# Performance work log

Measured on AMD Instinct MI355X. Metric: run time of the kernel, lower is better.

The kernel has to match this reference:

```python
import jax, jax.numpy as jnp
import numpy as np

E = 8            # num_experts
K = 2            # top-k
CF = 1.25        # capacity_factor
NOISE_STD = 1.0 / E   # noise_mult / num_experts


def setup_inputs() -> dict:
    key = jax.random.key(0)
    ks = jax.random.split(key, 4)
    B, S, D, H = 8, 1024, 768, 3072
    x = jax.random.normal(ks[0], (B, S, D), jnp.float32)
    router_w = jax.random.normal(ks[1], (D, E), jnp.float32) * 0.02
    fc1_w = jax.random.normal(ks[2], (E, D, H), jnp.float32) * 0.02
    fc1_b = jnp.zeros((E, H), jnp.float32)
    fc2_w = jax.random.normal(ks[3], (E, H, D), jnp.float32) * 0.02
    fc2_b = jnp.zeros((E, D), jnp.float32)
    return dict(x=x, router_w=router_w, fc1_w=fc1_w, fc1_b=fc1_b, fc2_w=fc2_w, fc2_b=fc2_b)


def reference(x, router_w, fc1_w, fc1_b, fc2_w, fc2_b):
    B, S, D = x.shape
    N = B * S
    A = N * K                                   # total (token, slot) assignments
    capacity = int(round(K * N * CF / E))
    x_flat = x.reshape(N, D)

    # ---- router (eval mode: no noise, no dropout) ----
    logits = (x_flat @ router_w).astype(jnp.float32)          # [N,E]
    clean_probs = jax.nn.softmax(logits, axis=-1)
    noisy_logits = logits
    noisy_probs = jax.nn.softmax(noisy_logits, axis=-1)
    topk_probs, topk_idx = jax.lax.top_k(noisy_probs, K)      # [N,K]
    topk_probs = topk_probs.astype(x.dtype)

    flat_e = topk_idx.reshape(-1)                             # [A]
    expert_counts = jax.ops.segment_sum(jnp.ones((A,), jnp.float32), flat_e, num_segments=E)

    # ---- aux losses ----
    importance = clean_probs.sum(0)
    mi = importance.mean()
    loss_importance = jnp.var(importance) / (mi * mi + 1e-6)
    # kthvalue(noisy_logits, E-K+1) == (E-K+1)-th smallest == sorted[:, E-K]
    threshold = jnp.sort(noisy_logits, axis=-1)[:, E - K][:, None]
    prob_selected = 1.0 - jax.scipy.stats.norm.cdf(threshold - logits, loc=0.0, scale=NOISE_STD)
    load = prob_selected.sum(0)
    ml = load.mean()
    loss_load = jnp.var(load) / (ml * ml + 1e-6)
    aux_loss = 0.5 * (loss_importance + loss_load)

    # ---- priority-based capacity dropping (vectorized over all assignments) ----
    priority = clean_probs.max(-1)                            # [N]
    tok = jnp.repeat(jnp.arange(N, dtype=jnp.int32), K)       # [A] token of each assignment
    kslot = jnp.tile(jnp.arange(K, dtype=jnp.int32), N)       # [A] which top-k slot
    score = priority[tok] - kslot.astype(jnp.float32)         # combined_scores = -k_idx + priority
    # group by expert (ascending), within expert sort by score descending
    sort_key = flat_e.astype(jnp.float32) * (K + 2) - score
    order = jnp.argsort(sort_key)
    e_sorted = flat_e[order]
    counts = jax.ops.segment_sum(jnp.ones((A,), jnp.int32), flat_e, num_segments=E)
    starts = jnp.cumsum(counts) - counts
    rank_sorted = jnp.arange(A, dtype=jnp.int32) - starts[e_sorted]   # position within expert group
    rank = jnp.zeros((A,), jnp.int32).at[order].set(rank_sorted)
    keep = rank < capacity
    dropped = jnp.sum(~keep).astype(jnp.int32)

    # ---- dispatch into fixed [E, capacity] buffer (overflow slot sliced off) ----
    pos = jnp.where(keep, flat_e * capacity + rank, E * capacity)
    dispatch_tok = jnp.zeros((E * capacity + 1,), jnp.int32).at[pos].set(tok)[:-1]
    w_flat = topk_probs.reshape(-1)
    weight_buf = jnp.zeros((E * capacity + 1,), x.dtype).at[pos].set(jnp.where(keep, w_flat, 0.0))[:-1]

    xe = x_flat[dispatch_tok].reshape(E, capacity, D)         # gather
    h = jax.nn.gelu(jnp.einsum('ecd,edh->ech', xe, fc1_w) + fc1_b[:, None, :], approximate=False)
    ye = jnp.einsum('ech,ehd->ecd', h, fc2_w) + fc2_b[:, None, :]
    weighted = ye * weight_buf.reshape(E, capacity, 1)
    # padded slots have weight 0 and token 0 -> contribute nothing
    out_flat = jnp.zeros((N, D), x.dtype).at[dispatch_tok].add(weighted.reshape(E * capacity, D))

    return out_flat.reshape(B, S, D), aux_loss, dropped, expert_counts
```

## Files before the change

### kernel.cpp

```cpp
#include <hip/hip_runtime.h>
#include <hip/hip_bf16.h>
#include <math.h>

#define NTOK 8192
#define DIM  768
#define HDIM 3072
#define NE   8
#define CAP  2560
#define AMAX 16384

typedef __bf16 bf16x8  __attribute__((ext_vector_type(8)));
typedef __bf16 bf16x2  __attribute__((ext_vector_type(2)));
typedef float  floatx4 __attribute__((ext_vector_type(4)));

typedef unsigned int u32_g __attribute__((address_space(1)));
typedef unsigned int u32_l __attribute__((address_space(3)));

__device__ __forceinline__ void gl_lds16(const void* g, void* l) {
  __builtin_amdgcn_global_load_lds((const u32_g*)g, (u32_l*)l, 16, 0, 0);
}

__device__ __forceinline__ float gelu_exact(float v) {
  float z = fabsf(v) * 0.7071067811865475f;
  float t = __builtin_amdgcn_rcpf(1.0f + 0.3275911f * z);
  float p = ((((1.061405429f * t - 1.453152027f) * t + 1.421413741f) * t
              - 0.284496736f) * t + 0.254829592f) * t;
  float e = 1.0f - p * __expf(-z * z);
  e = copysignf(e, v);
  return 0.5f * v * (1.0f + e);
}

__global__ __launch_bounds__(256) void transpose_conv2(
    const float* __restrict__ w1, const float* __restrict__ w2,
    __bf16* __restrict__ o1, __bf16* __restrict__ o2)
{
  const int which = blockIdx.z;
  const float* src = which ? w2 : w1;
  __bf16* dst = which ? o2 : o1;
  const int Kd = which ? HDIM : DIM;
  const int Nd = which ? DIM : HDIM;
  const int e = blockIdx.y;
  const int tilesK = Kd >> 6;
  const int bk = blockIdx.x % tilesK, bn = blockIdx.x / tilesK;
  __shared__ float T[64][65];
  const float* se = src + (size_t)e * Kd * Nd;
  const int k0 = bk * 64, n0 = bn * 64;
  const int tid = threadIdx.x;
#pragma unroll
  for (int it = 0; it < 16; ++it) {
    int flat = tid + it * 256;
    int kk = flat >> 6, nn = flat & 63;
    T[kk][nn] = se[(size_t)(k0 + kk) * Nd + n0 + nn];
  }
  __syncthreads();
  const int n = tid >> 2, kg = tid & 3;
  bf16x8 v0, v1;
#pragma unroll
  for (int q = 0; q < 8; ++q) v0[q] = (__bf16)T[kg * 16 + q][n];
#pragma unroll
  for (int q = 0; q < 8; ++q) v1[q] = (__bf16)T[kg * 16 + 8 + q][n];
  __bf16* de = dst + (size_t)e * Nd * Kd + (size_t)(n0 + n) * Kd + k0 + kg * 16;
  *(bf16x8*)(de) = v0;
  *(bf16x8*)(de + 8) = v1;
}

__global__ __launch_bounds__(256) void router_kernel(
    const float* __restrict__ x, const float* __restrict__ rw,
    int* __restrict__ list_len, double* __restrict__ imp, double* __restrict__ loadacc,
    int* __restrict__ aidx, float* __restrict__ keyarr, float* __restrict__ warr)
{
  __shared__ float Wl[NE * DIM];
  __shared__ int   lcount[NE], lbase[NE];
  __shared__ int   s_e[32][2], s_pos[32][2];
  __shared__ float s_key[32][2], s_w[32][2];
  const int tid = threadIdx.x;
  for (int i = tid; i < NE * DIM; i += 256) {
    int e = i / DIM, d = i - e * DIM;
    Wl[i] = rw[d * NE + e];
  }
  if (tid < NE) lcount[tid] = 0;
  __syncthreads();
  const int wave = tid >> 6, lane = tid & 63;
  double my_imp = 0.0, my_load = 0.0;

  for (int it = 0; it < 8; ++it) {
    const int t = wave * 8 + it;
    const int n = blockIdx.x * 32 + t;
    const float* xr = x + (size_t)n * DIM;
    float part[NE];
#pragma unroll
    for (int e = 0; e < NE; ++e) part[e] = 0.f;
#pragma unroll
    for (int c = 0; c < DIM / 64; ++c) {
      float xv = xr[c * 64 + lane];
#pragma unroll
      for (int e = 0; e < NE; ++e) part[e] += xv * Wl[e * DIM + c * 64 + lane];
    }
#pragma unroll
    for (int off = 32; off > 0; off >>= 1) {
#pragma unroll
      for (int e = 0; e < NE; ++e) part[e] += __shfl_xor(part[e], off);
    }
    int e0 = 0; float v0 = part[0];
#pragma unroll
    for (int e = 1; e < NE; ++e) if (part[e] > v0) { v0 = part[e]; e0 = e; }
    int e1 = -1; float v1 = -3.4e38f;
#pragma unroll
    for (int e = 0; e < NE; ++e) if (e != e0 && part[e] > v1) { v1 = part[e]; e1 = e; }

    float pexp[NE]; float s = 0.f;
#pragma unroll
    for (int e = 0; e < NE; ++e) { pexp[e] = expf(part[e] - v0); s += pexp[e]; }
    const float inv = 1.0f / s;
    const float pr = inv;
    float w1v = 0.f;
#pragma unroll
    for (int e = 0; e < NE; ++e) if (e == e1) w1v = pexp[e] * inv;

    float myl = 0.f, mypexp = 0.f;
#pragma unroll
    for (int e = 0; e < NE; ++e) if (lane == e) { myl = part[e]; mypexp = pexp[e]; }
    if (lane < NE) {
      my_imp  += (double)(mypexp * inv);
      my_load += (double)(0.5f * erfcf((v1 - myl) * 5.656854249492380f));
    }
    if (lane == 0) {
      int p0 = atomicAdd(&lcount[e0], 1);
      int p1 = atomicAdd(&lcount[e1], 1);
      s_e[t][0] = e0; s_pos[t][0] = p0;
      s_key[t][0] = (float)(e0 * 4) - pr;
      s_w[t][0] = pr;
      s_e[t][1] = e1; s_pos[t][1] = p1;
      s_key[t][1] = (float)(e1 * 4) - (pr - 1.0f);
      s_w[t][1] = w1v;
    }
  }
  __syncthreads();
  if (tid < NE) lbase[tid] = atomicAdd(&list_len[tid], lcount[tid]);
  __syncthreads();
  if (tid < 64) {
    const int t = tid >> 1, sl = tid & 1;
    const int e = s_e[t][sl];
    const int gp = lbase[e] + s_pos[t][sl];
    const int n = blockIdx.x * 32 + t;
    aidx[e * AMAX + gp]   = n * 2 + sl;
    keyarr[e * AMAX + gp] = s_key[t][sl];
    warr[e * AMAX + gp]   = s_w[t][sl];
  }
  if (lane < NE) {
    unsafeAtomicAdd(&imp[lane], my_imp);
    unsafeAtomicAdd(&loadacc[lane], my_load);
  }
}

__global__ __launch_bounds__(256) void compact_kernel(
    const int* __restrict__ list_len, const int* __restrict__ aidx,
    const float* __restrict__ keyarr, const float* __restrict__ warr,
    int* __restrict__ dtok, float* __restrict__ dw,
    const double* __restrict__ imp, const double* __restrict__ loadacc,
    float* __restrict__ out_scalars)
{
  __shared__ float sk[6144];
  __shared__ int   sa[6144];
  const int e = blockIdx.x, tid = threadIdx.x;
  const int C = list_len[e];
  if (C <= CAP) {
    for (int t = tid; t < C; t += 256) {
      int a = aidx[e * AMAX + t];
      dtok[e * CAP + t] = a >> 1;
      dw[e * CAP + t]   = warr[e * AMAX + t];
    }
  } else {
    const bool useL = (C <= 6144);
    if (useL) {
      for (int t = tid; t < C; t += 256) { sk[t] = keyarr[e*AMAX+t]; sa[t] = aidx[e*AMAX+t]; }
      __syncthreads();
    }
    for (int t = tid; t < C; t += 256) {
      float kt = keyarr[e*AMAX+t]; int at = aidx[e*AMAX+t];
      int r = 0;
      for (int u = 0; u < C; ++u) {
        float ku = useL ? sk[u] : keyarr[e*AMAX+u];
        int   au = useL ? sa[u] : aidx[e*AMAX+u];
        if (ku < kt || (ku == kt && au < at)) ++r;
      }
      if (r < CAP) { dtok[e*CAP + r] = at >> 1; dw[e*CAP + r] = warr[e*AMAX+t]; }
    }
  }
  if (e == 0 && tid == 0) {
    double mi = 0, ml = 0;
    for (int i = 0; i < NE; ++i) { mi += imp[i]; ml += loadacc[i]; }
    mi /= NE; ml /= NE;
    double vi = 0, vl = 0;
    for (int i = 0; i < NE; ++i) {
      double di = imp[i] - mi;     vi += di * di;
      double dl = loadacc[i] - ml; vl += dl * dl;
    }
    vi /= NE; vl /= NE;
    double li = vi / (mi * mi + 1e-6), ll = vl / (ml * ml + 1e-6);
    out_scalars[0] = (float)(0.5 * (li + ll));
    int drop = 0;
    for (int i = 0; i < NE; ++i) { int c2 = list_len[i]; if (c2 > CAP) drop += c2 - CAP; }
    out_scalars[1] = (float)drop;
    for (int i = 0; i < NE; ++i) out_scalars[2 + i] = (float)list_len[i];
  }
}

__global__ __launch_bounds__(256) void gather_kernel(
    const float* __restrict__ x, const int* __restrict__ dtok,
    const int* __restrict__ list_len, __bf16* __restrict__ Ag)
{
  const int row  = blockIdx.x * 4 + (threadIdx.x >> 6);
  const int lane = threadIdx.x & 63;
  const int e = row / CAP, slot = row - e * CAP;
  const int kept = min(list_len[e], CAP);
  __bf16* dst = Ag + (size_t)row * DIM;
  if (slot < kept) {
    const float* srcr = x + (size_t)dtok[e * CAP + slot] * DIM;
#pragma unroll
    for (int c = 0; c < DIM / 128; ++c) {
      float2 v = *(const float2*)(srcr + c * 128 + lane * 2);
      bf16x2 o; o[0] = (__bf16)v.x; o[1] = (__bf16)v.y;
      *(bf16x2*)(dst + c * 128 + lane * 2) = o;
    }
  } else {
    bf16x2 z; z[0] = (__bf16)0.f; z[1] = (__bf16)0.f;
#pragma unroll
    for (int c = 0; c < DIM / 128; ++c) *(bf16x2*)(dst + c * 128 + lane * 2) = z;
  }
}

#define BAR() do { asm volatile("" ::: "memory"); __builtin_amdgcn_s_barrier(); asm volatile("" ::: "memory"); } while (0)

#define ST_A(h, t, buf) do { \
    const __bf16* _g = gA[h] + (size_t)(t) * 64; \
    gl_lds16(_g,      &S[buf][((h) * 8 + wave) * 1024]); \
    gl_lds16(_g + 32, &S[buf][((h) * 8 + wave) * 1024 + 512]); \
  } while (0)

#define ST_B(h, t, buf) do { \
    const __bf16* _g = gB[h] + (size_t)(t) * 64; \
    gl_lds16(_g,      &S[buf][16384 + ((h) * 8 + wave) * 1024]); \
    gl_lds16(_g + 32, &S[buf][16384 + ((h) * 8 + wave) * 1024 + 512]); \
  } while (0)

#define RD_A(qm, buf) do { \
    _Pragma("unroll") \
    for (int _m = 0; _m < 4; ++_m) { \
      const int _g = wm * 8 + (qm) * 4 + _m; \
      aR[_m][0] = *(const bf16x8*)&S[buf][(_g * 2 + 0) * 512 + lane * 8]; \
      aR[_m][1] = *(const bf16x8*)&S[buf][(_g * 2 + 1) * 512 + lane * 8]; \
    } \
  } while (0)

#define RD_B(qn, buf) do { \
    _Pragma("unroll") \
    for (int _n = 0; _n < 2; ++_n) { \
      const int _g = wn * 4 + (qn) * 2 + _n; \
      bR[(qn) * 2 + _n][0] = *(const bf16x8*)&S[buf][16384 + (_g * 2 + 0) * 512 + lane * 8]; \
      bR[(qn) * 2 + _n][1] = *(const bf16x8*)&S[buf][16384 + (_g * 2 + 1) * 512 + lane * 8]; \
    } \
  } while (0)

#define MM(qm, qn) do { \
    __builtin_amdgcn_s_setprio(1); \
    _Pragma("unroll") \
    for (int _m = 0; _m < 4; ++_m) \
      _Pragma("unroll") \
      for (int _n = 0; _n < 2; ++_n) { \
        acc[(qm) * 4 + _m][(qn) * 2 + _n] = __builtin_amdgcn_mfma_f32_16x16x32_bf16( \
            aR[_m][0], bR[(qn) * 2 + _n][0], acc[(qm) * 4 + _m][(qn) * 2 + _n], 0, 0, 0); \
        acc[(qm) * 4 + _m][(qn) * 2 + _n] = __builtin_amdgcn_mfma_f32_16x16x32_bf16( \
            aR[_m][1], bR[(qn) * 2 + _n][1], acc[(qm) * 4 + _m][(qn) * 2 + _n], 0, 0, 0); \
      } \
    __builtin_amdgcn_s_setprio(0); \
  } while (0)

template<int MODE>
__global__ __launch_bounds__(512, 2) void moe_gemm8(
    const __bf16* __restrict__ Aall, const __bf16* __restrict__ BTall,
    const float* __restrict__ bias, __bf16* __restrict__ Hout,
    float* __restrict__ Out, const int* __restrict__ dtok, const float* __restrict__ dww,
    const int* __restrict__ list_len)
{
  const int Kd = MODE ? HDIM : DIM;
  const int Nd = MODE ? DIM : HDIM;
  const int numKt = Kd / 64;
  const int nIter = numKt / 2;

  const int i_blk = blockIdx.x;
  const int e = i_blk & 7;
  const int q = i_blk >> 3;
  const int tm = q % 10, tn = q / 10;

  const int kept = min(list_len[e], CAP);
  if (tm >= ((kept + 255) >> 8)) return;

  __shared__ __align__(16) __bf16 S[2][32768];

  const int tid = threadIdx.x, lane = tid & 63, wave = tid >> 6;
  const int wm = wave & 1, wn = wave >> 1;
  const int m0 = tm * 256, n0 = tn * 256;
  const int lr = lane & 15, kq = lane >> 4;

  const __bf16* Abase = Aall + (size_t)e * CAP * Kd;
  const __bf16* Bbase = BTall + (size_t)e * Nd * Kd;

  const __bf16* gA[2]; const __bf16* gB[2];
#pragma unroll
  for (int h = 0; h < 2; ++h) {
    gA[h] = Abase + (size_t)(m0 + (h * 8 + wave) * 16 + lr) * Kd + kq * 8;
    gB[h] = Bbase + (size_t)(n0 + (h * 8 + wave) * 16 + lr) * Kd + kq * 8;
  }

  floatx4 acc[8][4];
#pragma unroll
  for (int i = 0; i < 8; ++i)
#pragma unroll
    for (int j = 0; j < 4; ++j) acc[i][j] = (floatx4)0.f;

  bf16x8 aR[4][2], bR[4][2];

  ST_A(0, 0, 0); ST_A(1, 0, 0); ST_B(0, 0, 0); ST_B(1, 0, 0);
  ST_A(0, 1, 1);
  __builtin_amdgcn_s_waitcnt(0x0F72);
  BAR();

#pragma unroll 1
  for (int i = 0; i < nIter; ++i) {
    const int t0 = 2 * i;
    const bool more = (i < nIter - 1);

    RD_A(0, 0); RD_B(0, 0);
    ST_A(1, t0 + 1, 1);
    BAR(); MM(0, 0); BAR();
    RD_B(1, 0);
    ST_B(0, t0 + 1, 1);
    BAR(); MM(0, 1); BAR();
    RD_A(1, 0);
    ST_B(1, t0 + 1, 1);
    BAR(); MM(1, 1); BAR();
    if (more) {
      ST_A(0, t0 + 2, 0);
      __builtin_amdgcn_s_waitcnt(0x0F72);
    } else {
      __builtin_amdgcn_s_waitcnt(0x0F70);
    }
    BAR(); MM(1, 0); BAR();

    RD_A(0, 1); RD_B(0, 1);
    if (more) ST_A(1, t0 + 2, 0);
    BAR(); MM(0, 0); BAR();
    RD_B(1, 1);
    if (more) ST_B(0, t0 + 2, 0);
    BAR(); MM(0, 1); BAR();
    RD_A(1, 1);
    if (more) ST_B(1, t0 + 2, 0);
    BAR(); MM(1, 1); BAR();
    if (more) {
      ST_A(0, t0 + 3, 1);
      __builtin_amdgcn_s_waitcnt(0x0F72);
    } else {
      __builtin_amdgcn_s_waitcnt(0x0F70);
    }
    BAR(); MM(1, 0); BAR();
  }

  const int quad = lane >> 4, lcol = lane & 15;
  float bcol[4];
#pragma unroll
  for (int n = 0; n < 4; ++n)
    bcol[n] = bias[e * Nd + n0 + wn * 64 + n * 16 + lcol];

  if (MODE == 0) {
#pragma unroll
    for (int m = 0; m < 8; ++m) {
#pragma unroll
      for (int r = 0; r < 4; ++r) {
        const int row = m0 + wm * 128 + m * 16 + quad * 4 + r;
        __bf16* hrow = Hout + ((size_t)(e * CAP + row)) * Nd + n0 + wn * 64;
#pragma unroll
        for (int n = 0; n < 4; ++n)
          hrow[n * 16 + lcol] = (__bf16)gelu_exact(acc[m][n][r] + bcol[n]);
      }
    }
  } else {
#pragma unroll
    for (int m = 0; m < 8; ++m) {
#pragma unroll
      for (int r = 0; r < 4; ++r) {
        const int row = m0 + wm * 128 + m * 16 + quad * 4 + r;
        const float w = dww[e * CAP + row];
        if (w != 0.0f) {
          const int tok = dtok[e * CAP + row];
          float* orow = Out + (size_t)tok * DIM + n0 + wn * 64;
#pragma unroll
          for (int n = 0; n < 4; ++n)
            unsafeAtomicAdd(&orow[n * 16 + lcol], w * (acc[m][n][r] + bcol[n]));
        }
      }
    }
  }
}

#undef BAR
#undef ST_A
#undef ST_B
#undef RD_A
#undef RD_B
#undef MM

extern "C" void kernel_launch(void* const* d_in, const int* in_sizes, int n_in,
                              void* d_out, int out_size, void* d_ws, size_t ws_size,
                              hipStream_t stream) {
  (void)in_sizes; (void)n_in; (void)out_size; (void)ws_size;
  const float* x  = (const float*)d_in[0];
  const float* rw = (const float*)d_in[1];
  const float* w1 = (const float*)d_in[2];
  const float* b1 = (const float*)d_in[3];
  const float* w2 = (const float*)d_in[4];
  const float* b2 = (const float*)d_in[5];
  float* out = (float*)d_out;
  char* ws = (char*)d_ws;

  int*    list_len = (int*)(ws + 0);
  double* imp      = (double*)(ws + 64);
  double* loadacc  = (double*)(ws + 128);
  int*    dtok     = (int*)(ws + 256);
  float*  dw       = (float*)(ws + 256 + 81920);
  int*    aidx     = (int*)(ws + 164096);
  float*  keyarr   = (float*)(ws + 164096 + 524288);
  float*  warr     = (float*)(ws + 164096 + 1048576);
  __bf16* W1T      = (__bf16*)(ws + 2097152);
  __bf16* W2T      = (__bf16*)(ws + 2097152 + 37748736);
  __bf16* Ag       = (__bf16*)(ws + 2097152 + 2 * 37748736);
  __bf16* hbuf     = (__bf16*)(ws + 2097152 + 2 * 37748736 + 31457280);

  hipMemsetAsync(d_out, 0, (size_t)NTOK * DIM * sizeof(float), stream);
  hipMemsetAsync(ws, 0, 164096, stream);

  transpose_conv2<<<dim3(576, 8, 2), 256, 0, stream>>>(w1, w2, W1T, W2T);
  router_kernel<<<NTOK / 32, 256, 0, stream>>>(x, rw, list_len, imp, loadacc, aidx, keyarr, warr);
  compact_kernel<<<NE, 256, 0, stream>>>(list_len, aidx, keyarr, warr, dtok, dw, imp, loadacc,
                                         out + (size_t)NTOK * DIM);
  gather_kernel<<<(NE * CAP) / 4, 256, 0, stream>>>(x, dtok, list_len, Ag);
  moe_gemm8<0><<<NE * 10 * (HDIM / 256), 512, 0, stream>>>(
      Ag, W1T, b1, hbuf, nullptr, nullptr, nullptr, list_len);
  moe_gemm8<1><<<NE * 10 * (DIM / 256), 512, 0, stream>>>(
      hbuf, W2T, b2, nullptr, out, dtok, dw, list_len);
}
```

Baseline: 549.0 us.

## Restructure expert GEMM to 4-stage K=32 LDS pipeline

Replaces the 2-buffer, K=64 tile schedule with a 4-buffer ring of K=32 tiles, prefetching three tiles ahead through direct global-to-LDS loads. Each step now runs two MFMA phases with fewer barriers and a simpler wait-count scheme, plus an explicit epilogue that drains the last three tiles. The aim is deeper latency hiding of global loads and less barrier overhead per unit of math. The trade-off is half the MFMA work per barrier pair and more loop iterations.

```diff
diff --git a/kernel.cpp b/kernel.cpp
--- a/kernel.cpp
+++ b/kernel.cpp
@@ -232,47 +232,36 @@
 
 #define BAR() do { asm volatile("" ::: "memory"); __builtin_amdgcn_s_barrier(); asm volatile("" ::: "memory"); } while (0)
 
-#define ST_A(h, t, buf) do { \
-    const __bf16* _g = gA[h] + (size_t)(t) * 64; \
-    gl_lds16(_g,      &S[buf][((h) * 8 + wave) * 1024]); \
-    gl_lds16(_g + 32, &S[buf][((h) * 8 + wave) * 1024 + 512]); \
+#define ST_A(t, bf) do { \
+    gl_lds16(gA0 + (size_t)(t) * 32, &S[bf][(wave * 2 + 0) * 512]); \
+    gl_lds16(gA1 + (size_t)(t) * 32, &S[bf][(wave * 2 + 1) * 512]); \
   } while (0)
 
-#define ST_B(h, t, buf) do { \
-    const __bf16* _g = gB[h] + (size_t)(t) * 64; \
-    gl_lds16(_g,      &S[buf][16384 + ((h) * 8 + wave) * 1024]); \
-    gl_lds16(_g + 32, &S[buf][16384 + ((h) * 8 + wave) * 1024 + 512]); \
+#define ST_B(t, bf) do { \
+    gl_lds16(gB0 + (size_t)(t) * 32, &S[bf][8192 + (wave * 2 + 0) * 512]); \
+    gl_lds16(gB1 + (size_t)(t) * 32, &S[bf][8192 + (wave * 2 + 1) * 512]); \
   } while (0)
 
-#define RD_A(qm, buf) do { \
+#define RD_A(half, bf) do { \
     _Pragma("unroll") \
-    for (int _m = 0; _m < 4; ++_m) { \
-      const int _g = wm * 8 + (qm) * 4 + _m; \
-      aR[_m][0] = *(const bf16x8*)&S[buf][(_g * 2 + 0) * 512 + lane * 8]; \
-      aR[_m][1] = *(const bf16x8*)&S[buf][(_g * 2 + 1) * 512 + lane * 8]; \
-    } \
+    for (int _m = 0; _m < 4; ++_m) \
+      aR[_m] = *(const bf16x8*)&S[bf][(wm * 8 + (half) * 4 + _m) * 512 + lane * 8]; \
   } while (0)
 
-#define RD_B(qn, buf) do { \
+#define RD_B(bf) do { \
     _Pragma("unroll") \
-    for (int _n = 0; _n < 2; ++_n) { \
-      const int _g = wn * 4 + (qn) * 2 + _n; \
-      bR[(qn) * 2 + _n][0] = *(const bf16x8*)&S[buf][16384 + (_g * 2 + 0) * 512 + lane * 8]; \
-      bR[(qn) * 2 + _n][1] = *(const bf16x8*)&S[buf][16384 + (_g * 2 + 1) * 512 + lane * 8]; \
-    } \
+    for (int _n = 0; _n < 4; ++_n) \
+      bR[_n] = *(const bf16x8*)&S[bf][8192 + (wn * 4 + _n) * 512 + lane * 8]; \
   } while (0)
 
-#define MM(qm, qn) do { \
+#define MM(qm) do { \
     __builtin_amdgcn_s_setprio(1); \
     _Pragma("unroll") \
     for (int _m = 0; _m < 4; ++_m) \
       _Pragma("unroll") \
-      for (int _n = 0; _n < 2; ++_n) { \
-        acc[(qm) * 4 + _m][(qn) * 2 + _n] = __builtin_amdgcn_mfma_f32_16x16x32_bf16( \
-            aR[_m][0], bR[(qn) * 2 + _n][0], acc[(qm) * 4 + _m][(qn) * 2 + _n], 0, 0, 0); \
-        acc[(qm) * 4 + _m][(qn) * 2 + _n] = __builtin_amdgcn_mfma_f32_16x16x32_bf16( \
-            aR[_m][1], bR[(qn) * 2 + _n][1], acc[(qm) * 4 + _m][(qn) * 2 + _n], 0, 0, 0); \
-      } \
+      for (int _n = 0; _n < 4; ++_n) \
+        acc[(qm) * 4 + _m][_n] = __builtin_amdgcn_mfma_f32_16x16x32_bf16( \
+            aR[_m], bR[_n], acc[(qm) * 4 + _m][_n], 0, 0, 0); \
     __builtin_amdgcn_s_setprio(0); \
   } while (0)
 
@@ -285,8 +274,7 @@
 {
   const int Kd = MODE ? HDIM : DIM;
   const int Nd = MODE ? DIM : HDIM;
-  const int numKt = Kd / 64;
-  const int nIter = numKt / 2;
+  const int nT = Kd / 32;
 
   const int i_blk = blockIdx.x;
   const int e = i_blk & 7;
@@ -296,7 +284,7 @@
   const int kept = min(list_len[e], CAP);
   if (tm >= ((kept + 255) >> 8)) return;
 
-  __shared__ __align__(16) __bf16 S[2][32768];
+  __shared__ __align__(16) __bf16 S[4][16384];
 
   const int tid = threadIdx.x, lane = tid & 63, wave = tid >> 6;
   const int wm = wave & 1, wn = wave >> 1;
@@ -306,12 +294,10 @@
   const __bf16* Abase = Aall + (size_t)e * CAP * Kd;
   const __bf16* Bbase = BTall + (size_t)e * Nd * Kd;
 
-  const __bf16* gA[2]; const __bf16* gB[2];
-#pragma unroll
-  for (int h = 0; h < 2; ++h) {
-    gA[h] = Abase + (size_t)(m0 + (h * 8 + wave) * 16 + lr) * Kd + kq * 8;
-    gB[h] = Bbase + (size_t)(n0 + (h * 8 + wave) * 16 + lr) * Kd + kq * 8;
-  }
+  const __bf16* gA0 = Abase + (size_t)(m0 + (wave * 2 + 0) * 16 + lr) * Kd + kq * 8;
+  const __bf16* gA1 = Abase + (size_t)(m0 + (wave * 2 + 1) * 16 + lr) * Kd + kq * 8;
+  const __bf16* gB0 = Bbase + (size_t)(n0 + (wave * 2 + 0) * 16 + lr) * Kd + kq * 8;
+  const __bf16* gB1 = Bbase + (size_t)(n0 + (wave * 2 + 1) * 16 + lr) * Kd + kq * 8;
 
   floatx4 acc[8][4];
 #pragma unroll
@@ -319,51 +305,42 @@
 #pragma unroll
     for (int j = 0; j < 4; ++j) acc[i][j] = (floatx4)0.f;
 
-  bf16x8 aR[4][2], bR[4][2];
-
-  ST_A(0, 0, 0); ST_A(1, 0, 0); ST_B(0, 0, 0); ST_B(1, 0, 0);
-  ST_A(0, 1, 1);
-  __builtin_amdgcn_s_waitcnt(0x0F72);
+  bf16x8 aR[4], bR[4];
+
+  ST_A(0, 0); ST_B(0, 0);
+  ST_A(1, 1); ST_B(1, 1);
+  ST_A(2, 2); ST_B(2, 2);
+  __builtin_amdgcn_s_waitcnt(0x0F78);
   BAR();
 
 #pragma unroll 1
-  for (int i = 0; i < nIter; ++i) {
-    const int t0 = 2 * i;
-    const bool more = (i < nIter - 1);
-
-    RD_A(0, 0); RD_B(0, 0);
-    ST_A(1, t0 + 1, 1);
-    BAR(); MM(0, 0); BAR();
-    RD_B(1, 0);
-    ST_B(0, t0 + 1, 1);
-    BAR(); MM(0, 1); BAR();
-    RD_A(1, 0);
-    ST_B(1, t0 + 1, 1);
-    BAR(); MM(1, 1); BAR();
-    if (more) {
-      ST_A(0, t0 + 2, 0);
-      __builtin_amdgcn_s_waitcnt(0x0F72);
-    } else {
-      __builtin_amdgcn_s_waitcnt(0x0F70);
-    }
-    BAR(); MM(1, 0); BAR();
-
-    RD_A(0, 1); RD_B(0, 1);
-    if (more) ST_A(1, t0 + 2, 0);
-    BAR(); MM(0, 0); BAR();
-    RD_B(1, 1);
-    if (more) ST_B(0, t0 + 2, 0);
-    BAR(); MM(0, 1); BAR();
-    RD_A(1, 1);
-    if (more) ST_B(1, t0 + 2, 0);
-    BAR(); MM(1, 1); BAR();
-    if (more) {
-      ST_A(0, t0 + 3, 1);
-      __builtin_amdgcn_s_waitcnt(0x0F72);
-    } else {
-      __builtin_amdgcn_s_waitcnt(0x0F70);
-    }
-    BAR(); MM(1, 0); BAR();
+  for (int t = 0; t <= nT - 4; ++t) {
+    const int bt = t & 3, bs = (t + 3) & 3;
+    RD_A(0, bt); RD_B(bt);
+    ST_A(t + 3, bs);
+    BAR(); MM(0); BAR();
+    RD_A(1, bt);
+    ST_B(t + 3, bs);
+    __builtin_amdgcn_s_waitcnt(0x0F78);
+    BAR(); MM(1); BAR();
+  }
+
+  {
+    int bt = (nT - 3) & 3;
+    RD_A(0, bt); RD_B(bt); BAR(); MM(0); BAR();
+    RD_A(1, bt);
+    __builtin_amdgcn_s_waitcnt(0x0F74);
+    BAR(); MM(1); BAR();
+
+    bt = (nT - 2) & 3;
+    RD_A(0, bt); RD_B(bt); BAR(); MM(0); BAR();
+    RD_A(1, bt);
+    __builtin_amdgcn_s_waitcnt(0x0F70);
+    BAR(); MM(1); BAR();
+
+    bt = (nT - 1) & 3;
+    RD_A(0, bt); RD_B(bt); MM(0);
+    RD_A(1, bt); MM(1);
   }
 
   const int quad = lane >> 4, lcol = lane & 15;
```

Measured after the change: 533.4 us. 2.8% less time.
